# Optimization experiments

Measured on AMD Instinct MI355X. Metric: run time of the kernel, lower is better.

## Reference

```python
import jax, jax.numpy as jnp
import numpy as np

N_NODES = 20000
N_EDGES = 320000
IN_C = 256
HID = 32
HEADS0 = 4  # n_heads[0]: both #modules in first layer and heads per module
OUT_C = 40
NEG_SLOPE = 0.2


def _segment_softmax(e, seg, n):
    # e: [E, H], softmax over edges grouped by destination node
    m = jax.ops.segment_max(e, seg, num_segments=n)
    m = jnp.where(jnp.isfinite(m), m, 0.0)  # nodes with no in-edges
    ex = jnp.exp(e - m[seg])
    s = jax.ops.segment_sum(ex, seg, num_segments=n)
    return ex / (s[seg] + 1e-16)


def _gat_conv(x, W, a_src, a_dst, bias, src, dst, n, concat):
    # PyG GATConv math (self-loops assumed already appended to src/dst)
    H, C = a_src.shape
    h = (x @ W).reshape(n, H, C)                      # [N, H, C]
    e_src = (h * a_src).sum(-1)                       # [N, H]
    e_dst = (h * a_dst).sum(-1)                       # [N, H]
    e = jax.nn.leaky_relu(e_src[src] + e_dst[dst], NEG_SLOPE)  # [E, H]
    alpha = _segment_softmax(e, dst, n)               # [E, H]
    out = jax.ops.segment_sum(h[src] * alpha[:, :, None], dst, num_segments=n)
    if concat:
        return out.reshape(n, H * C) + bias
    return out.mean(axis=1) + bias


def setup_inputs() -> dict:
    key = jax.random.key(0)
    ks = jax.random.split(key, 12)
    x = jax.random.normal(ks[0], (N_NODES, IN_C), dtype=jnp.float32)
    edge_index = jax.random.randint(ks[1], (2, N_EDGES), 0, N_NODES, dtype=jnp.int32)
    M = HEADS0  # number of first-layer modules
    W1 = jax.random.normal(ks[2], (M, IN_C, HEADS0 * HID), dtype=jnp.float32) * 0.1
    a_src1 = jax.random.normal(ks[3], (M, HEADS0, HID), dtype=jnp.float32) * 0.1
    a_dst1 = jax.random.normal(ks[4], (M, HEADS0, HID), dtype=jnp.float32) * 0.1
    b1 = jax.random.normal(ks[5], (M, HEADS0 * HID), dtype=jnp.float32) * 0.1
    cat_dim = M * HEADS0 * HID  # 512: actual width after torch.cat over modules
    W2 = jax.random.normal(ks[6], (cat_dim, OUT_C), dtype=jnp.float32) * 0.1
    a_src2 = jax.random.normal(ks[7], (1, OUT_C), dtype=jnp.float32) * 0.1
    a_dst2 = jax.random.normal(ks[8], (1, OUT_C), dtype=jnp.float32) * 0.1
    b2 = jax.random.normal(ks[9], (OUT_C,), dtype=jnp.float32) * 0.1
    return {"x": x, "edge_index": edge_index, "W1": W1, "a_src1": a_src1,
            "a_dst1": a_dst1, "b1": b1, "W2": W2, "a_src2": a_src2,
            "a_dst2": a_dst2, "b2": b2}


def reference(x, edge_index, W1, a_src1, a_dst1, b1, W2, a_src2, a_dst2, b2):
    n = x.shape[0]
    loops = jnp.arange(n, dtype=edge_index.dtype)  # PyG add_self_loops=True
    src = jnp.concatenate([edge_index[0], loops])
    dst = jnp.concatenate([edge_index[1], loops])
    # first layer: HEADS0 independent GATConv modules, outputs concatenated
    outs = jax.vmap(lambda W, a_s, a_d, b: _gat_conv(x, W, a_s, a_d, b, src, dst, n, True))(
        W1, a_src1, a_dst1, b1)                      # [M, N, HEADS0*HID]
    h = jnp.transpose(outs, (1, 0, 2)).reshape(n, -1)  # [N, 512]
    h = jax.nn.elu(h)  # dropout is a no-op in eval mode
    out = _gat_conv(h, W2, a_src2, a_dst2, b2, src, dst, n, False)  # [N, OUT_C]
    return jax.nn.log_softmax(out, axis=1)
```

## Files before the change

kernel.cpp:

```cpp
#include <hip/hip_runtime.h>
#include <cstdint>
#include <cstddef>

#define N_NODES 20000
#define N_EDGES 320000
#define E_TOT   340000
#define IN_C    256
#define HID     32
#define HEADS0  4
#define OUT_C   40
#define NEG_SLOPE 0.2f
#define CAT     512
#define MH      16
#define H2S     48

typedef unsigned short ushort_t;
typedef __attribute__((ext_vector_type(8))) short short8v;
typedef __attribute__((ext_vector_type(4))) float f32x4;
typedef __attribute__((ext_vector_type(8))) unsigned short ushort8v;

#define WAVE_FENCE() asm volatile("" ::: "memory")

__device__ inline float bf2f(unsigned short u) {
  union { unsigned int i; float f; } c; c.i = ((unsigned int)u) << 16; return c.f;
}
__device__ inline unsigned short f2bf(float f) {
  union { float f; unsigned int i; } c; c.f = f;
  unsigned int r = c.i + 0x7FFFu + ((c.i >> 16) & 1u);
  return (unsigned short)(r >> 16);
}

#define DEGB ((E_TOT + 255) / 256)

__global__ __launch_bounds__(256) void prep_k(const float* __restrict__ W1,
                                              ushort_t* __restrict__ bhi,
                                              ushort_t* __restrict__ blo,
                                              const float* __restrict__ W2,
                                              ushort_t* __restrict__ b2hi,
                                              ushort_t* __restrict__ b2lo,
                                              const int* __restrict__ ei,
                                              int* __restrict__ deg) {
  int blk = blockIdx.x;
  if (blk < 64) {
    int idx = blk * 256 + threadIdx.x;
    int n16  = idx >> 9;
    int k32  = (idx >> 6) & 7;
    int lane = idx & 63;
    int cfull = n16 * 16 + (lane & 15);
    int m = cfull >> 7;
    int c = cfull & 127;
    int kbase = k32 * 32 + (lane >> 4) * 8;
#pragma unroll
    for (int b = 0; b < 8; b++) {
      float v = W1[((m << 8) + kbase + b) * 128 + c];
      ushort_t h = f2bf(v);
      bhi[(size_t)idx * 8 + b] = h;
      blo[(size_t)idx * 8 + b] = f2bf(v - bf2f(h));
    }
  } else if (blk < 76) {
    int idx = (blk - 64) * 256 + threadIdx.x;
    int n16  = idx >> 10;
    int k32  = (idx >> 6) & 15;
    int lane = idx & 63;
    int n = n16 * 16 + (lane & 15);
    int kbase = k32 * 32 + (lane >> 4) * 8;
#pragma unroll
    for (int b = 0; b < 8; b++) {
      float v = (n < OUT_C) ? W2[(kbase + b) * OUT_C + n] : 0.f;
      ushort_t h = f2bf(v);
      b2hi[(size_t)idx * 8 + b] = h;
      b2lo[(size_t)idx * 8 + b] = f2bf(v - bf2f(h));
    }
  } else {
    int e = (blk - 76) * 256 + threadIdx.x;
    if (e < E_TOT) {
      int d = (e < N_EDGES) ? ei[N_EDGES + e] : (e - N_EDGES);
      atomicAdd(&deg[d], 1);
    }
  }
}

__global__ __launch_bounds__(1024) void scan_k(const int* __restrict__ deg, int* __restrict__ row_ptr) {
  const int C = 20;
  __shared__ int part[1024];
  int t = threadIdx.x;
  int b = t * C;
  int s = 0;
  for (int i = 0; i < C; i++) { int idx = b + i; if (idx < N_NODES) s += deg[idx]; }
  part[t] = s;
  __syncthreads();
  for (int off = 1; off < 1024; off <<= 1) {
    int v = part[t];
    int u = (t >= off) ? part[t - off] : 0;
    __syncthreads();
    part[t] = v + u;
    __syncthreads();
  }
  int run = (t > 0) ? part[t - 1] : 0;
  for (int i = 0; i < C; i++) {
    int idx = b + i;
    if (idx <= N_NODES) {
      row_ptr[idx] = run;
      if (idx < N_NODES) run += deg[idx];
    }
  }
}

__global__ __launch_bounds__(256) void scatter_score_k(const int* __restrict__ ei,
                                                       const int* __restrict__ row_ptr,
                                                       int* __restrict__ fill,
                                                       int* __restrict__ csr_src,
                                                       const float* __restrict__ es1,
                                                       const float* __restrict__ ed1,
                                                       ushort_t* __restrict__ exq) {
  int e = blockIdx.x * 256 + threadIdx.x;
  if (e >= E_TOT) return;
  int s, d;
  if (e < N_EDGES) { s = ei[e]; d = ei[N_EDGES + e]; }
  else             { s = e - N_EDGES; d = s; }
  int pos = row_ptr[d] + atomicAdd(&fill[d], 1);
  csr_src[pos] = s;

  const float4* sp = (const float4*)(es1 + (size_t)s * MH);
  const float4* dp = (const float4*)(ed1 + (size_t)d * MH);
  float4 a0 = sp[0], a1 = sp[1], a2 = sp[2], a3 = sp[3];
  float4 b0 = dp[0], b1 = dp[1], b2 = dp[2], b3 = dp[3];
  float v[16] = {a0.x + b0.x, a0.y + b0.y, a0.z + b0.z, a0.w + b0.w,
                 a1.x + b1.x, a1.y + b1.y, a1.z + b1.z, a1.w + b1.w,
                 a2.x + b2.x, a2.y + b2.y, a2.z + b2.z, a2.w + b2.w,
                 a3.x + b3.x, a3.y + b3.y, a3.z + b3.z, a3.w + b3.w};
  ushort8v o0, o1;
#pragma unroll
  for (int i = 0; i < 16; i++) {
    float ev = v[i];
    ev = (ev > 0.f) ? ev : ev * NEG_SLOPE;
    float ex = __expf(ev);
    if (i < 8) o0[i] = f2bf(ex); else o1[i - 8] = f2bf(ex);
  }
  *(ushort8v*)(exq + (size_t)pos * MH)     = o0;
  *(ushort8v*)(exq + (size_t)pos * MH + 8) = o1;
}

__global__ __launch_bounds__(256) void gemm1_mfma_k(const float* __restrict__ x,
                                                    const ushort_t* __restrict__ bhi,
                                                    const ushort_t* __restrict__ blo,
                                                    const float* __restrict__ a_src1,
                                                    const float* __restrict__ a_dst1,
                                                    ushort_t* __restrict__ h1b,
                                                    float* __restrict__ es1,
                                                    float* __restrict__ ed1) {
  int tid = threadIdx.x;
  int wave = tid >> 6, lane = tid & 63;
  int l15 = lane & 15, lhi = lane >> 4;
  int wrow = blockIdx.x * 64 + (wave & 1) * 32;
  int wcol = blockIdx.y * 128 + (wave >> 1) * 64;
  int n16base = wcol >> 4;

  f32x4 acc[2][4];
#pragma unroll
  for (int mf = 0; mf < 2; mf++)
#pragma unroll
    for (int nf = 0; nf < 4; nf++) acc[mf][nf] = (f32x4){0.f, 0.f, 0.f, 0.f};

  int arow[2];
#pragma unroll
  for (int mf = 0; mf < 2; mf++) {
    int r = wrow + mf * 16 + l15;
    arow[mf] = (r < N_NODES) ? r : (N_NODES - 1);
  }

  for (int ks = 0; ks < 8; ks++) {
    short8v ah[2], al[2];
#pragma unroll
    for (int mf = 0; mf < 2; mf++) {
      const float4* xp = (const float4*)(x + (size_t)arow[mf] * IN_C + ks * 32 + lhi * 8);
      float4 f0 = xp[0], f1 = xp[1];
      float av8[8] = {f0.x, f0.y, f0.z, f0.w, f1.x, f1.y, f1.z, f1.w};
#pragma unroll
      for (int j = 0; j < 8; j++) {
        ushort_t h = f2bf(av8[j]);
        ah[mf][j] = (short)h;
        al[mf][j] = (short)f2bf(av8[j] - bf2f(h));
      }
    }
    short8v bh[4], bl[4];
#pragma unroll
    for (int nf = 0; nf < 4; nf++) {
      size_t off = ((size_t)((n16base + nf) * 8 + ks) * 64 + lane) * 8;
      bh[nf] = *(const short8v*)(bhi + off);
      bl[nf] = *(const short8v*)(blo + off);
    }
#pragma unroll
    for (int mf = 0; mf < 2; mf++)
#pragma unroll
      for (int nf = 0; nf < 4; nf++) {
        acc[mf][nf] = __builtin_amdgcn_mfma_f32_16x16x32_bf16(ah[mf], bh[nf], acc[mf][nf], 0, 0, 0);
        acc[mf][nf] = __builtin_amdgcn_mfma_f32_16x16x32_bf16(ah[mf], bl[nf], acc[mf][nf], 0, 0, 0);
        acc[mf][nf] = __builtin_amdgcn_mfma_f32_16x16x32_bf16(al[mf], bh[nf], acc[mf][nf], 0, 0, 0);
      }
  }

#pragma unroll
  for (int mf = 0; mf < 2; mf++) {
    int rbase = wrow + mf * 16 + lhi * 4;
#pragma unroll
    for (int nf = 0; nf < 4; nf++) {
      int col = wcol + nf * 16 + l15;
#pragma unroll
      for (int r = 0; r < 4; r++) {
        int row = rbase + r;
        if (row < N_NODES)
          h1b[(size_t)row * CAT + col] = f2bf(acc[mf][nf][r]);
      }
    }
  }

  int mh0 = wcol >> 5;
  float as[4], ad[4];
#pragma unroll
  for (int nf = 0; nf < 4; nf++) {
    int aidx = (mh0 + (nf >> 1)) * HID + (nf & 1) * 16 + l15;
    as[nf] = a_src1[aidx];
    ad[nf] = a_dst1[aidx];
  }
#pragma unroll
  for (int mf = 0; mf < 2; mf++) {
#pragma unroll
    for (int r = 0; r < 4; r++) {
      int row = wrow + mf * 16 + lhi * 4 + r;
      float ps0 = acc[mf][0][r] * as[0] + acc[mf][1][r] * as[1];
      float ps1 = acc[mf][2][r] * as[2] + acc[mf][3][r] * as[3];
      float pd0 = acc[mf][0][r] * ad[0] + acc[mf][1][r] * ad[1];
      float pd1 = acc[mf][2][r] * ad[2] + acc[mf][3][r] * ad[3];
#pragma unroll
      for (int msk = 1; msk < 16; msk <<= 1) {
        ps0 += __shfl_xor(ps0, msk); ps1 += __shfl_xor(ps1, msk);
        pd0 += __shfl_xor(pd0, msk); pd1 += __shfl_xor(pd1, msk);
      }
      if (l15 == 0 && row < N_NODES) {
        es1[row * MH + mh0]     = ps0;
        es1[row * MH + mh0 + 1] = ps1;
        ed1[row * MH + mh0]     = pd0;
        ed1[row * MH + mh0 + 1] = pd1;
      }
    }
  }
}


__global__ __launch_bounds__(256) void agg1_k(const ushort_t* __restrict__ h1b,
                                              const ushort_t* __restrict__ exq,
                                              const int* __restrict__ row_ptr,
                                              const int* __restrict__ csr_src,
                                              const float* __restrict__ b1,
                                              ushort_t* __restrict__ h1e) {
  int w = threadIdx.x >> 6, lane = threadIdx.x & 63;
  int n = blockIdx.x * 4 + w;
  int beg = row_ptr[n];
  int deg = row_ptr[n + 1] - beg;
  int hh = lane >> 2;

  __shared__ float ex_buf[4][64][MH + 1];
  __shared__ int   src_buf[4][64];

  float s_part[MH];
#pragma unroll
  for (int i = 0; i < MH; i++) s_part[i] = 0.f;
  float acc[8];
#pragma unroll
  for (int j = 0; j < 8; j++) acc[j] = 0.f;

  for (int base = 0; base < deg; base += 64) {
    int cnt = min(64, deg - base);
    if (lane < cnt) {
      int p = beg + base + lane;
      src_buf[w][lane] = csr_src[p];
      ushort8v q0 = *(const ushort8v*)(exq + (size_t)p * MH);
      ushort8v q1 = *(const ushort8v*)(exq + (size_t)p * MH + 8);
#pragma unroll
      for (int i = 0; i < 8; i++) {
        float ex = bf2f(q0[i]);
        ex_buf[w][lane][i] = ex;
        s_part[i] += ex;
      }
#pragma unroll
      for (int i = 0; i < 8; i++) {
        float ex = bf2f(q1[i]);
        ex_buf[w][lane][8 + i] = ex;
        s_part[8 + i] += ex;
      }
    }
    WAVE_FENCE();
    int e = 0;
    for (; e + 3 < cnt; e += 4) {
      int s0 = src_buf[w][e + 0], s1 = src_buf[w][e + 1];
      int s2 = src_buf[w][e + 2], s3 = src_buf[w][e + 3];
      float x0 = ex_buf[w][e + 0][hh], x1 = ex_buf[w][e + 1][hh];
      float x2 = ex_buf[w][e + 2][hh], x3 = ex_buf[w][e + 3][hh];
      ushort8v v0 = *(const ushort8v*)(h1b + (size_t)s0 * CAT + lane * 8);
      ushort8v v1 = *(const ushort8v*)(h1b + (size_t)s1 * CAT + lane * 8);
      ushort8v v2 = *(const ushort8v*)(h1b + (size_t)s2 * CAT + lane * 8);
      ushort8v v3 = *(const ushort8v*)(h1b + (size_t)s3 * CAT + lane * 8);
#pragma unroll
      for (int j = 0; j < 8; j++) acc[j] += x0 * bf2f(v0[j]);
#pragma unroll
      for (int j = 0; j < 8; j++) acc[j] += x1 * bf2f(v1[j]);
#pragma unroll
      for (int j = 0; j < 8; j++) acc[j] += x2 * bf2f(v2[j]);
#pragma unroll
      for (int j = 0; j < 8; j++) acc[j] += x3 * bf2f(v3[j]);
    }
    for (; e < cnt; e++) {
      int s = src_buf[w][e];
      float xv = ex_buf[w][e][hh];
      ushort8v hv = *(const ushort8v*)(h1b + (size_t)s * CAT + lane * 8);
#pragma unroll
      for (int j = 0; j < 8; j++) acc[j] += xv * bf2f(hv[j]);
    }
    WAVE_FENCE();
  }

  float denom = 0.f;
#pragma unroll
  for (int i = 0; i < MH; i++) {
    float v = s_part[i];
    v += __shfl_xor(v, 1);  v += __shfl_xor(v, 2);  v += __shfl_xor(v, 4);
    v += __shfl_xor(v, 8);  v += __shfl_xor(v, 16); v += __shfl_xor(v, 32);
    if (hh == i) denom = v;
  }
  denom += 1e-16f;

  const float4* b1p = (const float4*)(b1 + lane * 8);
  float4 bq0 = b1p[0], bq1 = b1p[1];
  float bv8[8] = {bq0.x, bq0.y, bq0.z, bq0.w, bq1.x, bq1.y, bq1.z, bq1.w};

  ushort8v vhi;
#pragma unroll
  for (int j = 0; j < 8; j++) {
    float o = acc[j] / denom + bv8[j];
    float e = (o > 0.f) ? o : (__expf(o) - 1.f);
    vhi[j] = f2bf(e);
  }
  *(ushort8v*)(h1e + (size_t)n * CAT + lane * 8) = vhi;
}

__global__ __launch_bounds__(256) void gemm2_mfma_k(const ushort_t* __restrict__ h1e,
                                                    const ushort_t* __restrict__ b2hi,
                                                    const ushort_t* __restrict__ b2lo,
                                                    const float* __restrict__ a_src2,
                                                    const float* __restrict__ a_dst2,
                                                    ushort_t* __restrict__ h2b,
                                                    float* __restrict__ es2,
                                                    float* __restrict__ ed2) {
  int tid = threadIdx.x;
  int wave = tid >> 6, lane = tid & 63;
  int l15 = lane & 15, lhi = lane >> 4;
  int wrow = blockIdx.x * 64 + wave * 16;

  f32x4 acc[3];
#pragma unroll
  for (int nf = 0; nf < 3; nf++) acc[nf] = (f32x4){0.f, 0.f, 0.f, 0.f};

  int r0 = wrow + l15;
  int arow = (r0 < N_NODES) ? r0 : (N_NODES - 1);

  for (int ks = 0; ks < 16; ks++) {
    size_t aoff = (size_t)arow * CAT + ks * 32 + lhi * 8;
    short8v ah = *(const short8v*)(h1e + aoff);
#pragma unroll
    for (int nf = 0; nf < 3; nf++) {
      size_t boff = ((size_t)(nf * 16 + ks) * 64 + lane) * 8;
      short8v bh = *(const short8v*)(b2hi + boff);
      short8v bl = *(const short8v*)(b2lo + boff);
      acc[nf] = __builtin_amdgcn_mfma_f32_16x16x32_bf16(ah, bh, acc[nf], 0, 0, 0);
      acc[nf] = __builtin_amdgcn_mfma_f32_16x16x32_bf16(ah, bl, acc[nf], 0, 0, 0);
    }
  }

  float av[3], bv[3];
#pragma unroll
  for (int nf = 0; nf < 3; nf++) {
    int col = nf * 16 + l15;
    av[nf] = (col < OUT_C) ? a_src2[col] : 0.f;
    bv[nf] = (col < OUT_C) ? a_dst2[col] : 0.f;
  }
#pragma unroll
  for (int r = 0; r < 4; r++) {
    int row = wrow + lhi * 4 + r;
    float ps = acc[0][r] * av[0] + acc[1][r] * av[1] + acc[2][r] * av[2];
    float pd = acc[0][r] * bv[0] + acc[1][r] * bv[1] + acc[2][r] * bv[2];
    ps += __shfl_xor(ps, 1); pd += __shfl_xor(pd, 1);
    ps += __shfl_xor(ps, 2); pd += __shfl_xor(pd, 2);
    ps += __shfl_xor(ps, 4); pd += __shfl_xor(pd, 4);
    ps += __shfl_xor(ps, 8); pd += __shfl_xor(pd, 8);
    if (row < N_NODES) {
#pragma unroll
      for (int nf = 0; nf < 3; nf++)
        h2b[(size_t)row * H2S + nf * 16 + l15] = f2bf(acc[nf][r]);
      if (l15 == 0) { es2[row] = ps; ed2[row] = pd; }
    }
  }
}

__global__ __launch_bounds__(256) void agg2_k(const ushort_t* __restrict__ h2b,
                                              const float* __restrict__ es2,
                                              const float* __restrict__ ed2,
                                              const int* __restrict__ row_ptr,
                                              const int* __restrict__ csr_src,
                                              const float* __restrict__ b2,
                                              float* __restrict__ out) {
  int w = threadIdx.x >> 6, lane = threadIdx.x & 63;
  int n = blockIdx.x * 4 + w;
  int beg = row_ptr[n];
  int deg = row_ptr[n + 1] - beg;
  float edn = ed2[n];

  __shared__ float exb[4][64];
  __shared__ int   srb[4][64];

  float acc = 0.f, ssum = 0.f;
  for (int base = 0; base < deg; base += 64) {
    int cnt = min(64, deg - base);
    if (lane < cnt) {
      int s = csr_src[beg + base + lane];
      srb[w][lane] = s;
      float ev = es2[s] + edn;
      ev = (ev > 0.f) ? ev : ev * NEG_SLOPE;
      float ex = __expf(ev);
      exb[w][lane] = ex;
      ssum += ex;
    }
    WAVE_FENCE();
    int e = 0;
    for (; e + 3 < cnt; e += 4) {
      int s0 = srb[w][e], s1 = srb[w][e + 1], s2 = srb[w][e + 2], s3 = srb[w][e + 3];
      float x0 = exb[w][e], x1 = exb[w][e + 1], x2 = exb[w][e + 2], x3 = exb[w][e + 3];
      if (lane < OUT_C) {
        float v0 = bf2f(h2b[(size_t)s0 * H2S + lane]);
        float v1 = bf2f(h2b[(size_t)s1 * H2S + lane]);
        float v2 = bf2f(h2b[(size_t)s2 * H2S + lane]);
        float v3 = bf2f(h2b[(size_t)s3 * H2S + lane]);
        acc += x0 * v0; acc += x1 * v1; acc += x2 * v2; acc += x3 * v3;
      }
    }
    for (; e < cnt; e++) {
      int s = srb[w][e];
      float xv = exb[w][e];
      if (lane < OUT_C) acc += xv * bf2f(h2b[(size_t)s * H2S + lane]);
    }
    WAVE_FENCE();
  }

  ssum += __shfl_xor(ssum, 1); ssum += __shfl_xor(ssum, 2); ssum += __shfl_xor(ssum, 4);
  ssum += __shfl_xor(ssum, 8); ssum += __shfl_xor(ssum, 16); ssum += __shfl_xor(ssum, 32);

  float val = (lane < OUT_C) ? (acc / (ssum + 1e-16f) + b2[lane]) : -INFINITY;

  float rmax = val;
#pragma unroll
  for (int o = 1; o < 64; o <<= 1) rmax = fmaxf(rmax, __shfl_xor(rmax, o));
  float ex = (lane < OUT_C) ? __expf(val - rmax) : 0.f;
  float sume = ex;
#pragma unroll
  for (int o = 1; o < 64; o <<= 1) sume += __shfl_xor(sume, o);
  if (lane < OUT_C) out[(size_t)n * OUT_C + lane] = val - rmax - __logf(sume);
}


extern "C" void kernel_launch(void* const* d_in, const int* in_sizes, int n_in,
                              void* d_out, int out_size, void* d_ws, size_t ws_size,
                              hipStream_t stream) {
  const float* x      = (const float*)d_in[0];
  const int*   ei     = (const int*)d_in[1];
  const float* W1     = (const float*)d_in[2];
  const float* a_src1 = (const float*)d_in[3];
  const float* a_dst1 = (const float*)d_in[4];
  const float* b1     = (const float*)d_in[5];
  const float* W2     = (const float*)d_in[6];
  const float* a_src2 = (const float*)d_in[7];
  const float* a_dst2 = (const float*)d_in[8];
  const float* b2     = (const float*)d_in[9];
  float* out = (float*)d_out;

  char* ws = (char*)d_ws;
  size_t off = 0;
  auto alloc = [&](size_t bytes) -> void* {
    void* p = ws + off;
    off += (bytes + 255) & ~(size_t)255;
    return p;
  };
  ushort_t* bhi  = (ushort_t*)alloc((size_t)32 * 8 * 64 * 8 * 2);
  ushort_t* blo  = (ushort_t*)alloc((size_t)32 * 8 * 64 * 8 * 2);
  ushort_t* b2hi = (ushort_t*)alloc((size_t)3 * 16 * 64 * 8 * 2);
  ushort_t* b2lo = (ushort_t*)alloc((size_t)3 * 16 * 64 * 8 * 2);
  ushort_t* h1b  = (ushort_t*)alloc((size_t)N_NODES * CAT * 2);
  ushort_t* h1e  = (ushort_t*)alloc((size_t)N_NODES * CAT * 2);
  ushort_t* exq  = (ushort_t*)alloc((size_t)E_TOT * MH * 2);
  float* es1     = (float*)alloc((size_t)N_NODES * MH * 4);
  float* ed1     = (float*)alloc((size_t)N_NODES * MH * 4);
  ushort_t* h2b  = (ushort_t*)alloc((size_t)N_NODES * H2S * 2);
  float* es2     = (float*)alloc((size_t)N_NODES * 4);
  float* ed2     = (float*)alloc((size_t)N_NODES * 4);
  int*   deg     = (int*)alloc((size_t)N_NODES * 4);
  int*   fill    = (int*)alloc((size_t)N_NODES * 4);
  int*   row_ptr = (int*)alloc((size_t)(N_NODES + 1) * 4);
  int*   csr_src = (int*)alloc((size_t)E_TOT * 4);

  hipMemsetAsync(deg, 0, (((size_t)N_NODES * 4 + 255) & ~(size_t)255) + (size_t)N_NODES * 4, stream);

  prep_k<<<64 + 12 + DEGB, 256, 0, stream>>>(W1, bhi, blo, W2, b2hi, b2lo, ei, deg);
  scan_k<<<1, 1024, 0, stream>>>(deg, row_ptr);
  gemm1_mfma_k<<<dim3((N_NODES + 63) / 64, CAT / 128), 256, 0, stream>>>(
      x, bhi, blo, a_src1, a_dst1, h1b, es1, ed1);
  scatter_score_k<<<(E_TOT + 255) / 256, 256, 0, stream>>>(
      ei, row_ptr, fill, csr_src, es1, ed1, exq);
  agg1_k<<<N_NODES / 4, 256, 0, stream>>>(h1b, exq, row_ptr, csr_src, b1, h1e);
  gemm2_mfma_k<<<(N_NODES + 63) / 64, 256, 0, stream>>>(h1e, b2hi, b2lo, a_src2, a_dst2, h2b, es2, ed2);
  agg2_k<<<N_NODES / 4, 256, 0, stream>>>(h2b, es2, ed2, row_ptr, csr_src, b2, out);
}
```

Baseline: 193.1 us.

## Retile first GEMM to full-width rows per block and drop x low-part MFMA

The first-layer GEMM now gives each block 32 rows and all 512 output columns, with each wave owning 128 columns (4 module-heads). The x tile is therefore loaded and converted to bf16 once per row block rather than once per column block. The low-order bf16 correction term for x is removed, cutting the MFMA count per tile from three to two. Row bounds checks are dropped because 20000 divides evenly by 32. The trade-offs are lower precision in the x@W1 product and more accumulator registers per wave, which may reduce occupancy.

After: 226.7 us. +17.4%, slower.

```diff
diff --git a/kernel.cpp b/kernel.cpp
--- a/kernel.cpp
+++ b/kernel.cpp
@@ -152,74 +152,57 @@
   int tid = threadIdx.x;
   int wave = tid >> 6, lane = tid & 63;
   int l15 = lane & 15, lhi = lane >> 4;
-  int wrow = blockIdx.x * 64 + (wave & 1) * 32;
-  int wcol = blockIdx.y * 128 + (wave >> 1) * 64;
-  int n16base = wcol >> 4;
-
-  f32x4 acc[2][4];
+  int wrow = blockIdx.x * 32;
+  int n16base = wave * 8;
+
+  f32x4 acc[2][8];
 #pragma unroll
   for (int mf = 0; mf < 2; mf++)
 #pragma unroll
-    for (int nf = 0; nf < 4; nf++) acc[mf][nf] = (f32x4){0.f, 0.f, 0.f, 0.f};
+    for (int nf = 0; nf < 8; nf++) acc[mf][nf] = (f32x4){0.f, 0.f, 0.f, 0.f};
 
   int arow[2];
 #pragma unroll
-  for (int mf = 0; mf < 2; mf++) {
-    int r = wrow + mf * 16 + l15;
-    arow[mf] = (r < N_NODES) ? r : (N_NODES - 1);
-  }
+  for (int mf = 0; mf < 2; mf++) arow[mf] = wrow + mf * 16 + l15;
 
   for (int ks = 0; ks < 8; ks++) {
-    short8v ah[2], al[2];
+    short8v ah[2];
 #pragma unroll
     for (int mf = 0; mf < 2; mf++) {
       const float4* xp = (const float4*)(x + (size_t)arow[mf] * IN_C + ks * 32 + lhi * 8);
       float4 f0 = xp[0], f1 = xp[1];
       float av8[8] = {f0.x, f0.y, f0.z, f0.w, f1.x, f1.y, f1.z, f1.w};
 #pragma unroll
-      for (int j = 0; j < 8; j++) {
-        ushort_t h = f2bf(av8[j]);
-        ah[mf][j] = (short)h;
-        al[mf][j] = (short)f2bf(av8[j] - bf2f(h));
-      }
-    }
-    short8v bh[4], bl[4];
-#pragma unroll
-    for (int nf = 0; nf < 4; nf++) {
-      size_t off = ((size_t)((n16base + nf) * 8 + ks) * 64 + lane) * 8;
-      bh[nf] = *(const short8v*)(bhi + off);
-      bl[nf] = *(const short8v*)(blo + off);
-    }
-#pragma unroll
-    for (int mf = 0; mf < 2; mf++)
-#pragma unroll
-      for (int nf = 0; nf < 4; nf++) {
-        acc[mf][nf] = __builtin_amdgcn_mfma_f32_16x16x32_bf16(ah[mf], bh[nf], acc[mf][nf], 0, 0, 0);
-        acc[mf][nf] = __builtin_amdgcn_mfma_f32_16x16x32_bf16(ah[mf], bl[nf], acc[mf][nf], 0, 0, 0);
-        acc[mf][nf] = __builtin_amdgcn_mfma_f32_16x16x32_bf16(al[mf], bh[nf], acc[mf][nf], 0, 0, 0);
-      }
+      for (int j = 0; j < 8; j++) ah[mf][j] = (short)f2bf(av8[j]);
+    }
+#pragma unroll
+    for (int nf = 0; nf < 8; nf++) {
+      size_t boff = ((size_t)((n16base + nf) * 8 + ks) * 64 + lane) * 8;
+      short8v bh = *(const short8v*)(bhi + boff);
+      short8v bl = *(const short8v*)(blo + boff);
+      acc[0][nf] = __builtin_amdgcn_mfma_f32_16x16x32_bf16(ah[0], bh, acc[0][nf], 0, 0, 0);
+      acc[1][nf] = __builtin_amdgcn_mfma_f32_16x16x32_bf16(ah[1], bh, acc[1][nf], 0, 0, 0);
+      acc[0][nf] = __builtin_amdgcn_mfma_f32_16x16x32_bf16(ah[0], bl, acc[0][nf], 0, 0, 0);
+      acc[1][nf] = __builtin_amdgcn_mfma_f32_16x16x32_bf16(ah[1], bl, acc[1][nf], 0, 0, 0);
+    }
   }
 
 #pragma unroll
   for (int mf = 0; mf < 2; mf++) {
     int rbase = wrow + mf * 16 + lhi * 4;
 #pragma unroll
-    for (int nf = 0; nf < 4; nf++) {
-      int col = wcol + nf * 16 + l15;
-#pragma unroll
-      for (int r = 0; r < 4; r++) {
-        int row = rbase + r;
-        if (row < N_NODES)
-          h1b[(size_t)row * CAT + col] = f2bf(acc[mf][nf][r]);
-      }
-    }
-  }
-
-  int mh0 = wcol >> 5;
-  float as[4], ad[4];
-#pragma unroll
-  for (int nf = 0; nf < 4; nf++) {
-    int aidx = (mh0 + (nf >> 1)) * HID + (nf & 1) * 16 + l15;
+    for (int nf = 0; nf < 8; nf++) {
+      int col = wave * 128 + nf * 16 + l15;
+#pragma unroll
+      for (int r = 0; r < 4; r++)
+        h1b[(size_t)(rbase + r) * CAT + col] = f2bf(acc[mf][nf][r]);
+    }
+  }
+
+  float as[8], ad[8];
+#pragma unroll
+  for (int nf = 0; nf < 8; nf++) {
+    int aidx = (wave * 4 + (nf >> 1)) * HID + (nf & 1) * 16 + l15;
     as[nf] = a_src1[aidx];
     ad[nf] = a_dst1[aidx];
   }
@@ -228,20 +211,26 @@
 #pragma unroll
     for (int r = 0; r < 4; r++) {
       int row = wrow + mf * 16 + lhi * 4 + r;
-      float ps0 = acc[mf][0][r] * as[0] + acc[mf][1][r] * as[1];
-      float ps1 = acc[mf][2][r] * as[2] + acc[mf][3][r] * as[3];
-      float pd0 = acc[mf][0][r] * ad[0] + acc[mf][1][r] * ad[1];
-      float pd1 = acc[mf][2][r] * ad[2] + acc[mf][3][r] * ad[3];
+      float ps[4], pd[4];
+#pragma unroll
+      for (int h = 0; h < 4; h++) {
+        ps[h] = acc[mf][2 * h][r] * as[2 * h] + acc[mf][2 * h + 1][r] * as[2 * h + 1];
+        pd[h] = acc[mf][2 * h][r] * ad[2 * h] + acc[mf][2 * h + 1][r] * ad[2 * h + 1];
+      }
 #pragma unroll
       for (int msk = 1; msk < 16; msk <<= 1) {
-        ps0 += __shfl_xor(ps0, msk); ps1 += __shfl_xor(ps1, msk);
-        pd0 += __shfl_xor(pd0, msk); pd1 += __shfl_xor(pd1, msk);
+#pragma unroll
+        for (int h = 0; h < 4; h++) {
+          ps[h] += __shfl_xor(ps[h], msk);
+          pd[h] += __shfl_xor(pd[h], msk);
+        }
       }
-      if (l15 == 0 && row < N_NODES) {
-        es1[row * MH + mh0]     = ps0;
-        es1[row * MH + mh0 + 1] = ps1;
-        ed1[row * MH + mh0]     = pd0;
-        ed1[row * MH + mh0 + 1] = pd1;
+      if (l15 == 0) {
+#pragma unroll
+        for (int h = 0; h < 4; h++) {
+          es1[row * MH + wave * 4 + h] = ps[h];
+          ed1[row * MH + wave * 4 + h] = pd[h];
+        }
       }
     }
   }
@@ -510,7 +499,7 @@
 
   prep_k<<<64 + 12 + DEGB, 256, 0, stream>>>(W1, bhi, blo, W2, b2hi, b2lo, ei, deg);
   scan_k<<<1, 1024, 0, stream>>>(deg, row_ptr);
-  gemm1_mfma_k<<<dim3((N_NODES + 63) / 64, CAT / 128), 256, 0, stream>>>(
+  gemm1_mfma_k<<<N_NODES / 32, 256, 0, stream>>>(
       x, bhi, blo, a_src1, a_dst1, h1b, es1, ed1);
   scatter_score_k<<<(E_TOT + 255) / 256, 256, 0, stream>>>(
       ei, row_ptr, fill, csr_src, es1, ed1, exq);
```
